# Performance work log

Hardware: AMD Instinct MI355X
Metric: run time of the kernel (lower is better)

## Reference

```python
import jax, jax.numpy as jnp
import numpy as np

NUM_NODES = 20000
LOOKBACK = 7
DAYS = 4
NUM_FEATURES = 5
HIDDEN = 128
NUM_EDGES = 320000


def setup_inputs() -> dict:
    key = jax.random.key(0)
    ks = jax.random.split(key, 10)
    p = lambda k, shape: jax.random.normal(k, shape, dtype=jnp.float32) * 0.1
    return {
        "x": jax.random.normal(ks[0], (DAYS * NUM_NODES, LOOKBACK, NUM_FEATURES), dtype=jnp.float32),
        "edge_index": jax.random.randint(ks[1], (2, NUM_EDGES), 0, NUM_NODES, dtype=jnp.int32),
        "W1": p(ks[2], (NUM_FEATURES, HIDDEN)),
        "b1": jnp.zeros((HIDDEN,), jnp.float32),
        "W2": p(ks[3], (HIDDEN, HIDDEN)),
        "b2": jnp.zeros((HIDDEN,), jnp.float32),
        "W_ih": p(ks[4], (3 * HIDDEN, HIDDEN)),
        "W_hh": p(ks[5], (3 * HIDDEN, HIDDEN)),
        "b_ih": jnp.zeros((3 * HIDDEN,), jnp.float32),
        "b_hh": jnp.zeros((3 * HIDDEN,), jnp.float32),
        "W_out": p(ks[6], (HIDDEN, 5)),
        "b_out": jnp.zeros((5,), jnp.float32),
    }


def reference(x, edge_index, W1, b1, W2, b2, W_ih, W_hh, b_ih, b_hh, W_out, b_out):
    # Eval mode: dropout is identity.
    src, dst = edge_index[0], edge_index[1]
    # GCN symmetric normalization with self-loops: deg includes the self-loop (+1).
    deg = jax.ops.segment_sum(jnp.ones((NUM_EDGES,), jnp.float32), dst, num_segments=NUM_NODES) + 1.0
    dinv = jax.lax.rsqrt(deg)                      # [N]
    norm_e = dinv[src] * dinv[dst]                 # [E] edge norm
    self_norm = 1.0 / deg                          # [N] self-loop norm

    def gcn(h_in, W, b):
        h = h_in @ W                               # [N, C_out]
        msg = h[src] * norm_e[:, None]             # gather + scale  [E, C_out]
        agg = jax.ops.segment_sum(msg, dst, num_segments=NUM_NODES)
        return agg + h * self_norm[:, None] + b

    def gru(xt, h):
        gi = xt @ W_ih.T + b_ih
        gh = h @ W_hh.T + b_hh
        i_r, i_z, i_n = jnp.split(gi, 3, axis=1)
        h_r, h_z, h_n = jnp.split(gh, 3, axis=1)
        r = jax.nn.sigmoid(i_r + h_r)
        z = jax.nn.sigmoid(i_z + h_z)
        n = jnp.tanh(i_n + r * h_n)
        return (1.0 - z) * n + z * h

    def day_fwd(x_day):  # x_day: [N, lookback, F]
        def step(h, xt):
            z1 = jax.nn.relu(gcn(xt, W1, b1))
            z2 = jax.nn.relu(gcn(z1, W2, b2))
            return gru(z2, h), None
        h0 = jnp.zeros((NUM_NODES, HIDDEN), jnp.float32)
        hT, _ = jax.lax.scan(step, h0, jnp.swapaxes(x_day, 0, 1))  # scan over lookback
        return jax.nn.softmax(hT @ W_out + b_out, axis=1)          # [N, 5]

    x_days = x.reshape(DAYS, NUM_NODES, LOOKBACK, NUM_FEATURES)
    out = jax.vmap(day_fwd)(x_days)                # [DAYS, N, 5]
    return out.reshape(DAYS * NUM_NODES, 5)
```

## Files before the change

### kernel.cpp

```cpp
#include <hip/hip_runtime.h>
#include <cstddef>
#include <cstdint>

#define N_NODES 20000
#define N_EDGES 320000
#define NDAYS 4
#define LOOKBACK 7
#define NFEAT 5
#define XROW (LOOKBACK * NFEAT)
#define HIDDEN 128
#define GRUROWS 32

typedef short bf8 __attribute__((ext_vector_type(8)));
typedef float fx4 __attribute__((ext_vector_type(4)));

__device__ __forceinline__ float bflo(unsigned int u) {
    union { unsigned int u; float f; } v; v.u = u << 16; return v.f;
}
__device__ __forceinline__ float bfhi(unsigned int u) {
    union { unsigned int u; float f; } v; v.u = u & 0xffff0000u; return v.f;
}
__device__ __forceinline__ unsigned short f2bf(float f) {
    union { float f; unsigned int u; } v; v.f = f;
    unsigned int u = v.u + 0x7fffu + ((v.u >> 16) & 1u);
    return (unsigned short)(u >> 16);
}
__device__ __forceinline__ unsigned int packbf(float a, float b) {
    return (unsigned int)f2bf(a) | ((unsigned int)f2bf(b) << 16);
}
__device__ __forceinline__ float sigm(float v) { return 1.0f / (1.0f + __expf(-v)); }
__device__ __forceinline__ float ftanh(float v) {
    float e2 = __expf(2.0f * v);
    return (e2 - 1.0f) / (e2 + 1.0f);
}
__device__ __forceinline__ void accum8(float* a, uint4 v, float w) {
    a[0] += w * bflo(v.x); a[1] += w * bfhi(v.x);
    a[2] += w * bflo(v.y); a[3] += w * bfhi(v.y);
    a[4] += w * bflo(v.z); a[5] += w * bfhi(v.z);
    a[6] += w * bflo(v.w); a[7] += w * bfhi(v.w);
}


__global__ __launch_bounds__(256) void k_deg(const int* __restrict__ ei, int* __restrict__ deg) {
    int e = blockIdx.x * 256 + threadIdx.x;
    if (e < N_EDGES) atomicAdd(&deg[ei[N_EDGES + e]], 1);
}

__global__ __launch_bounds__(1024) void k_scan(const int* __restrict__ deg, int* __restrict__ row_start) {
    __shared__ int part[1024];
    int tid = threadIdx.x;
    const int chunk = (N_NODES + 1023) / 1024;
    int i0 = tid * chunk;
    int i1 = min(i0 + chunk, N_NODES);
    int s = 0;
    for (int i = i0; i < i1; ++i) s += deg[i];
    part[tid] = s;
    __syncthreads();
    for (int d = 1; d < 1024; d <<= 1) {
        int v = (tid >= d) ? part[tid - d] : 0;
        __syncthreads();
        part[tid] += v;
        __syncthreads();
    }
    int base = part[tid] - s;
    for (int i = i0; i < i1; ++i) { row_start[i] = base; base += deg[i]; }
    if (tid == 1023) row_start[N_NODES] = part[1023];
}

__global__ __launch_bounds__(256) void k_dinv(const int* __restrict__ deg, float* __restrict__ dinv,
                                              float* __restrict__ self_norm) {
    int i = blockIdx.x * 256 + threadIdx.x;
    if (i >= N_NODES) return;
    float d = (float)(deg[i] + 1);
    dinv[i] = 1.0f / sqrtf(d);
    self_norm[i] = 1.0f / d;
}

__global__ __launch_bounds__(256) void k_fill(const int* __restrict__ ei, const int* __restrict__ row_start,
                                              int* __restrict__ cursor, const float* __restrict__ dinv,
                                              int* __restrict__ csr_src, float* __restrict__ csr_norm) {
    int e = blockIdx.x * 256 + threadIdx.x;
    if (e >= N_EDGES) return;
    int s = ei[e], d = ei[N_EDGES + e];
    int pos = row_start[d] + atomicAdd(&cursor[d], 1);
    csr_src[pos] = s;
    csr_norm[pos] = dinv[s] * dinv[d];
}

__global__ __launch_bounds__(256) void k_w2t(const float* __restrict__ W2, unsigned short* __restrict__ W2T) {
    int idx = blockIdx.x * 256 + threadIdx.x;
    if (idx >= HIDDEN * HIDDEN) return;
    int k = idx >> 7, c = idx & 127;
    W2T[c * HIDDEN + k] = f2bf(W2[k * HIDDEN + c]);
}

__global__ __launch_bounds__(256) void k_cast(const float* __restrict__ src, unsigned short* __restrict__ dst, int n) {
    int i = blockIdx.x * 256 + threadIdx.x;
    if (i < n) dst[i] = f2bf(src[i]);
}

__global__ __launch_bounds__(256) void k_bfold(const float* __restrict__ b_ih, const float* __restrict__ b_hh,
                                               float* __restrict__ b_fold) {
    int i = blockIdx.x * 256 + threadIdx.x;
    if (i < 3 * HIDDEN) b_fold[i] = b_ih[i] + (i < 2 * HIDDEN ? b_hh[i] : 0.0f);
}


template<int NB>
__global__ __launch_bounds__(256) void k_aggx(const float* __restrict__ x, float* __restrict__ xa,
                                              const int* __restrict__ row_start, const int* __restrict__ csr_src,
                                              const float* __restrict__ csr_norm,
                                              const float* __restrict__ self_norm, int dayBase) {
    int n = blockIdx.x * 4 + (threadIdx.x >> 6);
    if (n >= N_NODES) return;
    int lane = threadIdx.x & 63;
    if (lane >= XROW) return;
    float sn = self_norm[n];
    float acc[NB];
#pragma unroll
    for (int b = 0; b < NB; ++b)
        acc[b] = x[(size_t)((dayBase + b) * N_NODES + n) * XROW + lane] * sn;
    int e1 = row_start[n + 1];
    for (int e = row_start[n]; e < e1; ++e) {
        int s = csr_src[e];
        float w = csr_norm[e];
#pragma unroll
        for (int b = 0; b < NB; ++b)
            acc[b] += w * x[(size_t)((dayBase + b) * N_NODES + s) * XROW + lane];
    }
#pragma unroll
    for (int b = 0; b < NB; ++b)
        xa[(size_t)(n * NB + b) * XROW + lane] = acc[b];
}


__global__ __launch_bounds__(256) void k_z1gemm(const float* __restrict__ xa, const float* __restrict__ W1,
                                                const float* __restrict__ b1,
                                                const unsigned short* __restrict__ W2T,
                                                unsigned short* __restrict__ H2, int rows, int t) {
    int tid = threadIdx.x, w = tid >> 6, l = tid & 63, lr = l & 15, lk = l >> 4;
    int rblk = blockIdx.x * 64;
    int rowA = rblk + w * 16 + lr;
    bool okA = rowA < rows;
    float x5[5];
#pragma unroll
    for (int k = 0; k < 5; ++k)
        x5[k] = okA ? xa[(size_t)rowA * XROW + t * NFEAT + k] : 0.0f;
    bf8 az[4];
#pragma unroll
    for (int ks = 0; ks < 4; ++ks) {
#pragma unroll
        for (int j = 0; j < 8; ++j) {
            int ch = 32 * ks + 8 * lk + j;
            float v = b1[ch] + x5[0] * W1[ch] + x5[1] * W1[128 + ch] + x5[2] * W1[256 + ch]
                    + x5[3] * W1[384 + ch] + x5[4] * W1[512 + ch];
            az[ks][j] = (short)f2bf(fmaxf(v, 0.0f));
        }
    }
    const bf8* Bp = (const bf8*)W2T;
    fx4 acc[8];
#pragma unroll
    for (int n = 0; n < 8; ++n) acc[n] = (fx4){0.f, 0.f, 0.f, 0.f};
#pragma unroll
    for (int ks = 0; ks < 4; ++ks) {
#pragma unroll
        for (int n = 0; n < 8; ++n) {
            bf8 b = Bp[(size_t)(16 * n + lr) * 16 + 4 * ks + lk];
            acc[n] = __builtin_amdgcn_mfma_f32_16x16x32_bf16(az[ks], b, acc[n], 0, 0, 0);
        }
    }
#pragma unroll
    for (int n = 0; n < 8; ++n)
#pragma unroll
        for (int r = 0; r < 4; ++r) {
            int row = rblk + w * 16 + lk * 4 + r;
            if (row < rows) H2[(size_t)row * HIDDEN + 16 * n + lr] = f2bf(acc[n][r]);
        }
}


template<int NB>
__global__ __launch_bounds__(256) void k_agg(const uint4* __restrict__ H, uint4* __restrict__ Z,
                                             const float* __restrict__ bias,
                                             const int* __restrict__ row_start, const int* __restrict__ csr_src,
                                             const float* __restrict__ csr_norm,
                                             const float* __restrict__ self_norm) {
    int n = blockIdx.x * 4 + (threadIdx.x >> 6);
    if (n >= N_NODES) return;
    int l = threadIdx.x & 63;
    if (l >= NB * 16) return;
    int c0 = (l & 15) * 8;
    float sn = self_norm[n];
    float a[8];
    {
        uint4 sv = H[(size_t)n * (NB * 16) + l];
        a[0] = bflo(sv.x) * sn; a[1] = bfhi(sv.x) * sn;
        a[2] = bflo(sv.y) * sn; a[3] = bfhi(sv.y) * sn;
        a[4] = bflo(sv.z) * sn; a[5] = bfhi(sv.z) * sn;
        a[6] = bflo(sv.w) * sn; a[7] = bfhi(sv.w) * sn;
    }
    int e1 = row_start[n + 1];
    int e = row_start[n];
    for (; e + 3 < e1; e += 4) {
        int s0 = csr_src[e], s1 = csr_src[e + 1], s2 = csr_src[e + 2], s3 = csr_src[e + 3];
        float w0 = csr_norm[e], w1 = csr_norm[e + 1], w2 = csr_norm[e + 2], w3 = csr_norm[e + 3];
        uint4 v0 = H[(size_t)s0 * (NB * 16) + l];
        uint4 v1 = H[(size_t)s1 * (NB * 16) + l];
        uint4 v2 = H[(size_t)s2 * (NB * 16) + l];
        uint4 v3 = H[(size_t)s3 * (NB * 16) + l];
        accum8(a, v0, w0); accum8(a, v1, w1); accum8(a, v2, w2); accum8(a, v3, w3);
    }
    for (; e < e1; ++e) {
        int s = csr_src[e];
        float w = csr_norm[e];
        uint4 v = H[(size_t)s * (NB * 16) + l];
        accum8(a, v, w);
    }
    const float* bp = bias + c0;
    uint4 o;
    o.x = packbf(fmaxf(a[0] + bp[0], 0.f), fmaxf(a[1] + bp[1], 0.f));
    o.y = packbf(fmaxf(a[2] + bp[2], 0.f), fmaxf(a[3] + bp[3], 0.f));
    o.z = packbf(fmaxf(a[4] + bp[4], 0.f), fmaxf(a[5] + bp[5], 0.f));
    o.w = packbf(fmaxf(a[6] + bp[6], 0.f), fmaxf(a[7] + bp[7], 0.f));
    Z[(size_t)n * (NB * 16) + l] = o;
}


template<bool FIRST>
__global__ __launch_bounds__(512, 1) void k_megagru(const unsigned short* __restrict__ Z2all,
                                                    float* __restrict__ Hf,
                                                    const unsigned short* __restrict__ Wih,
                                                    const unsigned short* __restrict__ Whh,
                                                    const float* __restrict__ bfold,
                                                    const float* __restrict__ bhh, int rows, int NT) {
    __shared__ __align__(16) char hlds[2 * GRUROWS * 256];
    __shared__ __align__(16) char wlds[384 * 256];
    const int HALF = GRUROWS * 256;
    int tid = threadIdx.x, w = tid >> 6, l = tid & 63, lr = l & 15, lk = l >> 4;
    int row0 = blockIdx.x * GRUROWS;
    int c = w * 16 + lr;

    {
        const uint4* wsrc = (const uint4*)Whh;
        for (int i = tid; i < 384 * 16; i += 512) {
            int rw = i >> 4, chunk = i & 15;
            uint4 v = wsrc[(size_t)rw * 16 + chunk];
            int byte = rw * 256 + ((chunk * 16) ^ ((rw & 15) << 4));
            *(uint4*)(wlds + byte) = v;
        }
    }

    bf8 Bi[3][4];
    const bf8* BiP = (const bf8*)Wih;
#pragma unroll
    for (int g = 0; g < 3; ++g)
#pragma unroll
        for (int ks = 0; ks < 4; ++ks)
            Bi[g][ks] = BiP[(size_t)(g * HIDDEN + c) * 16 + 4 * ks + lk];

    float bf_r = bfold[c], bf_z = bfold[HIDDEN + c], bf_n = bfold[2 * HIDDEN + c];
    float bh_n = bhh[2 * HIDDEN + c];

    float hreg[2][4];
    if (FIRST) {
#pragma unroll
        for (int m = 0; m < 2; ++m)
#pragma unroll
            for (int r = 0; r < 4; ++r) hreg[m][r] = 0.f;
        for (int i = tid; i < HALF / 4; i += 512) ((unsigned int*)hlds)[i] = 0u;
    } else {
#pragma unroll
        for (int m = 0; m < 2; ++m)
#pragma unroll
            for (int r = 0; r < 4; ++r) {
                int row = 16 * m + lk * 4 + r;
                float h = Hf[(size_t)(row0 + row) * HIDDEN + c];
                hreg[m][r] = h;
                int byte = row * 256 + ((c * 2) ^ ((row & 15) << 4));
                *(unsigned short*)(hlds + byte) = f2bf(h);
            }
    }
    __syncthreads();

    for (int t = 0; t < NT; ++t) {
        const int p = t & 1;
        const unsigned short* z2t = Z2all + ((size_t)t * rows + row0) * HIDDEN;
#pragma unroll
        for (int m = 0; m < 2; ++m) {
            bf8 az[4];
            const bf8* zp = (const bf8*)(z2t + (size_t)(16 * m + lr) * HIDDEN);
#pragma unroll
            for (int ks = 0; ks < 4; ++ks) az[ks] = zp[4 * ks + lk];
            bf8 ah[4];
#pragma unroll
            for (int ks = 0; ks < 4; ++ks) {
                int byte = p * HALF + (16 * m + lr) * 256 + ((ks * 64 + lk * 16) ^ (lr << 4));
                ah[ks] = *(const bf8*)(hlds + byte);
            }
            fx4 aR = (fx4){0.f, 0.f, 0.f, 0.f};
            fx4 aZ = (fx4){0.f, 0.f, 0.f, 0.f};
            fx4 aNi = (fx4){0.f, 0.f, 0.f, 0.f};
            fx4 aNh = (fx4){0.f, 0.f, 0.f, 0.f};
#pragma unroll
            for (int ks = 0; ks < 4; ++ks) {
                int wb = (ks * 64 + lk * 16) ^ (lr << 4);
                bf8 bhR = *(const bf8*)(wlds + (0 * HIDDEN + c) * 256 + wb);
                bf8 bhZ = *(const bf8*)(wlds + (1 * HIDDEN + c) * 256 + wb);
                bf8 bhN = *(const bf8*)(wlds + (2 * HIDDEN + c) * 256 + wb);
                aR = __builtin_amdgcn_mfma_f32_16x16x32_bf16(ah[ks], bhR, aR, 0, 0, 0);
                aZ = __builtin_amdgcn_mfma_f32_16x16x32_bf16(ah[ks], bhZ, aZ, 0, 0, 0);
                aNh = __builtin_amdgcn_mfma_f32_16x16x32_bf16(ah[ks], bhN, aNh, 0, 0, 0);
            }
#pragma unroll
            for (int ks = 0; ks < 4; ++ks) {
                aR = __builtin_amdgcn_mfma_f32_16x16x32_bf16(az[ks], Bi[0][ks], aR, 0, 0, 0);
                aZ = __builtin_amdgcn_mfma_f32_16x16x32_bf16(az[ks], Bi[1][ks], aZ, 0, 0, 0);
                aNi = __builtin_amdgcn_mfma_f32_16x16x32_bf16(az[ks], Bi[2][ks], aNi, 0, 0, 0);
            }
#pragma unroll
            for (int r = 0; r < 4; ++r) {
                int row = 16 * m + lk * 4 + r;
                float rr = sigm(aR[r] + bf_r);
                float zz = sigm(aZ[r] + bf_z);
                float nn = ftanh(aNi[r] + bf_n + rr * (aNh[r] + bh_n));
                float hnew = (1.0f - zz) * nn + zz * hreg[m][r];
                hreg[m][r] = hnew;
                int byte = (p ^ 1) * HALF + row * 256 + ((c * 2) ^ ((row & 15) << 4));
                *(unsigned short*)(hlds + byte) = f2bf(hnew);
            }
        }
        asm volatile("s_waitcnt lgkmcnt(0)" ::: "memory");
        __builtin_amdgcn_s_barrier();
        __builtin_amdgcn_sched_barrier(0);
    }

#pragma unroll
    for (int m = 0; m < 2; ++m)
#pragma unroll
        for (int r = 0; r < 4; ++r)
            Hf[(size_t)(row0 + 16 * m + lk * 4 + r) * HIDDEN + c] = hreg[m][r];
}


template<int NB>
__global__ __launch_bounds__(256) void k_out(const float* __restrict__ Hc, const float* __restrict__ Wo,
                                             const float* __restrict__ bo, float* __restrict__ out,
                                             int dayBase) {
    int rr = blockIdx.x * 4 + (threadIdx.x >> 6);
    if (rr >= N_NODES * NB) return;
    int lane = threadIdx.x & 63;
    float2 hv = ((const float2*)(Hc + (size_t)rr * HIDDEN))[lane];
    float l[5];
#pragma unroll
    for (int j = 0; j < 5; ++j) {
        float p = hv.x * Wo[(2 * lane) * 5 + j] + hv.y * Wo[(2 * lane + 1) * 5 + j];
#pragma unroll
        for (int s = 1; s < 64; s <<= 1) p += __shfl_xor(p, s);
        l[j] = p + bo[j];
    }
    float m = fmaxf(fmaxf(fmaxf(l[0], l[1]), fmaxf(l[2], l[3])), l[4]);
    float e0 = expf(l[0] - m), e1 = expf(l[1] - m), e2 = expf(l[2] - m), e3 = expf(l[3] - m), e4 = expf(l[4] - m);
    float inv = 1.0f / (e0 + e1 + e2 + e3 + e4);
    if (lane < 5) {
        float ej = lane == 0 ? e0 : lane == 1 ? e1 : lane == 2 ? e2 : lane == 3 ? e3 : e4;
        int n = rr / NB, dd = dayBase + rr % NB;
        out[((size_t)dd * N_NODES + n) * 5 + lane] = ej * inv;
    }
}


template<int NB>
static void run_tier(const float* x, const float* W1, const float* b1,
                     const unsigned short* W2T_bf, const float* b2,
                     const unsigned short* Wih_bf, const unsigned short* Whh_bf,
                     const float* b_fold, const float* b_hh,
                     const float* W_out, const float* b_out, float* out,
                     const int* row_start, const int* csr_src, const float* csr_norm,
                     const float* self_norm,
                     float* xa, unsigned short* H2, unsigned short* Z2all, float* Hf,
                     hipStream_t stream) {
    const int rows = N_NODES * NB;
    const unsigned ngrid = (N_NODES + 3) / 4;
    const unsigned gblk = (unsigned)((rows + 63) / 64);
    const unsigned gru_grid = (unsigned)(rows / GRUROWS);
    const int rounds = NDAYS / NB;
    for (int dd = 0; dd < rounds; ++dd) {
        int dayBase = dd * NB;
        k_aggx<NB><<<ngrid, 256, 0, stream>>>(x, xa, row_start, csr_src, csr_norm, self_norm, dayBase);
        for (int t = 0; t < 4; ++t) {
            k_z1gemm<<<gblk, 256, 0, stream>>>(xa, W1, b1, W2T_bf, H2, rows, t);
            k_agg<NB><<<ngrid, 256, 0, stream>>>((const uint4*)H2,
                                                 (uint4*)(Z2all + (size_t)t * rows * HIDDEN), b2,
                                                 row_start, csr_src, csr_norm, self_norm);
        }
        k_megagru<true><<<gru_grid, 512, 0, stream>>>(Z2all, Hf, Wih_bf, Whh_bf, b_fold, b_hh, rows, 4);
        for (int t = 4; t < LOOKBACK; ++t) {
            k_z1gemm<<<gblk, 256, 0, stream>>>(xa, W1, b1, W2T_bf, H2, rows, t);
            k_agg<NB><<<ngrid, 256, 0, stream>>>((const uint4*)H2,
                                                 (uint4*)(Z2all + (size_t)(t - 4) * rows * HIDDEN), b2,
                                                 row_start, csr_src, csr_norm, self_norm);
        }
        k_megagru<false><<<gru_grid, 512, 0, stream>>>(Z2all, Hf, Wih_bf, Whh_bf, b_fold, b_hh, rows, 3);
        k_out<NB><<<(unsigned)((rows + 3) / 4), 256, 0, stream>>>(Hf, W_out, b_out, out, dayBase);
    }
}


extern "C" void kernel_launch(void* const* d_in, const int* in_sizes, int n_in,
                              void* d_out, int out_size, void* d_ws, size_t ws_size,
                              hipStream_t stream) {
    const float* x     = (const float*)d_in[0];
    const int*   ei    = (const int*)d_in[1];
    const float* W1    = (const float*)d_in[2];
    const float* b1    = (const float*)d_in[3];
    const float* W2    = (const float*)d_in[4];
    const float* b2    = (const float*)d_in[5];
    const float* W_ih  = (const float*)d_in[6];
    const float* W_hh  = (const float*)d_in[7];
    const float* b_ih  = (const float*)d_in[8];
    const float* b_hh  = (const float*)d_in[9];
    const float* W_out = (const float*)d_in[10];
    const float* b_out = (const float*)d_in[11];
    float* out = (float*)d_out;

    size_t off = 0;
    char* wsb = (char*)d_ws;
    auto alloc = [&](size_t bytes) -> void* {
        void* p = wsb + off;
        off = (off + bytes + 255) & ~(size_t)255;
        return p;
    };
    int*            deg       = (int*)alloc(N_NODES * 4);
    int*            cursor    = (int*)alloc(N_NODES * 4);
    int*            row_start = (int*)alloc((N_NODES + 1) * 4);
    float*          dinv      = (float*)alloc(N_NODES * 4);
    float*          self_norm = (float*)alloc(N_NODES * 4);
    unsigned short* W2T_bf    = (unsigned short*)alloc(HIDDEN * HIDDEN * 2);
    unsigned short* Wih_bf    = (unsigned short*)alloc(3 * HIDDEN * HIDDEN * 2);
    unsigned short* Whh_bf    = (unsigned short*)alloc(3 * HIDDEN * HIDDEN * 2);
    float*          b_fold    = (float*)alloc(3 * HIDDEN * 4);
    int*            csr_src   = (int*)alloc(N_EDGES * 4);
    float*          csr_norm  = (float*)alloc(N_EDGES * 4);

    size_t prep_off = off;
    auto need = [&](int nb) -> size_t {
        return prep_off + (size_t)N_NODES * nb * 1932 + 16384;
    };
    int NBsel = (need(4) <= ws_size) ? 4 : (need(2) <= ws_size) ? 2 : 1;
    int rows = N_NODES * NBsel;

    float*          xa    = (float*)alloc((size_t)rows * XROW * 4);
    unsigned short* H2    = (unsigned short*)alloc((size_t)rows * HIDDEN * 2);
    unsigned short* Z2all = (unsigned short*)alloc((size_t)4 * rows * HIDDEN * 2);
    float*          Hf    = (float*)alloc((size_t)rows * HIDDEN * 4);

    hipMemsetAsync(deg, 0, N_NODES * 4, stream);
    hipMemsetAsync(cursor, 0, N_NODES * 4, stream);
    k_deg<<<(N_EDGES + 255) / 256, 256, 0, stream>>>(ei, deg);
    k_scan<<<1, 1024, 0, stream>>>(deg, row_start);
    k_dinv<<<(N_NODES + 255) / 256, 256, 0, stream>>>(deg, dinv, self_norm);
    k_fill<<<(N_EDGES + 255) / 256, 256, 0, stream>>>(ei, row_start, cursor, dinv, csr_src, csr_norm);
    k_w2t<<<(HIDDEN * HIDDEN + 255) / 256, 256, 0, stream>>>(W2, W2T_bf);
    k_cast<<<(3 * HIDDEN * HIDDEN + 255) / 256, 256, 0, stream>>>(W_ih, Wih_bf, 3 * HIDDEN * HIDDEN);
    k_cast<<<(3 * HIDDEN * HIDDEN + 255) / 256, 256, 0, stream>>>(W_hh, Whh_bf, 3 * HIDDEN * HIDDEN);
    k_bfold<<<2, 256, 0, stream>>>(b_ih, b_hh, b_fold);

    if (NBsel == 4)
        run_tier<4>(x, W1, b1, W2T_bf, b2, Wih_bf, Whh_bf, b_fold, b_hh, W_out, b_out, out,
                    row_start, csr_src, csr_norm, self_norm, xa, H2, Z2all, Hf, stream);
    else if (NBsel == 2)
        run_tier<2>(x, W1, b1, W2T_bf, b2, Wih_bf, Whh_bf, b_fold, b_hh, W_out, b_out, out,
                    row_start, csr_src, csr_norm, self_norm, xa, H2, Z2all, Hf, stream);
    else
        run_tier<1>(x, W1, b1, W2T_bf, b2, Wih_bf, Whh_bf, b_fold, b_hh, W_out, b_out, out,
                    row_start, csr_src, csr_norm, self_norm, xa, H2, Z2all, Hf, stream);
}
```

Before: 1.096 ms.

## Double GRU rows per block and hoist W_hh LDS fragments out of row loop

The fused GRU kernel now processes 64 rows per block instead of 32, with bounds guards for a partial last block. The recurrent-weight fragments are read from LDS once per timestep and reused across all four 16-row tiles instead of being reloaded per tile. This cuts LDS traffic and amortizes the per-block W_hh staging, but it raises register pressure (more hreg and 12 extra bf8 fragments) and halves the block count, which may reduce occupancy.

```diff
diff --git a/kernel.cpp b/kernel.cpp
--- a/kernel.cpp
+++ b/kernel.cpp
@@ -9,7 +9,7 @@
 #define NFEAT 5
 #define XROW (LOOKBACK * NFEAT)
 #define HIDDEN 128
-#define GRUROWS 32
+#define GRUROWS 64
 
 typedef short bf8 __attribute__((ext_vector_type(8)));
 typedef float fx4 __attribute__((ext_vector_type(4)));
@@ -261,20 +261,21 @@
     float bf_r = bfold[c], bf_z = bfold[HIDDEN + c], bf_n = bfold[2 * HIDDEN + c];
     float bh_n = bhh[2 * HIDDEN + c];
 
-    float hreg[2][4];
+    float hreg[4][4];
     if (FIRST) {
 #pragma unroll
-        for (int m = 0; m < 2; ++m)
+        for (int m = 0; m < 4; ++m)
 #pragma unroll
             for (int r = 0; r < 4; ++r) hreg[m][r] = 0.f;
         for (int i = tid; i < HALF / 4; i += 512) ((unsigned int*)hlds)[i] = 0u;
     } else {
 #pragma unroll
-        for (int m = 0; m < 2; ++m)
+        for (int m = 0; m < 4; ++m)
 #pragma unroll
             for (int r = 0; r < 4; ++r) {
                 int row = 16 * m + lk * 4 + r;
-                float h = Hf[(size_t)(row0 + row) * HIDDEN + c];
+                int grow = row0 + row;
+                float h = (grow < rows) ? Hf[(size_t)grow * HIDDEN + c] : 0.0f;
                 hreg[m][r] = h;
                 int byte = row * 256 + ((c * 2) ^ ((row & 15) << 4));
                 *(unsigned short*)(hlds + byte) = f2bf(h);
@@ -285,12 +286,25 @@
     for (int t = 0; t < NT; ++t) {
         const int p = t & 1;
         const unsigned short* z2t = Z2all + ((size_t)t * rows + row0) * HIDDEN;
-#pragma unroll
-        for (int m = 0; m < 2; ++m) {
+
+        bf8 bwR[4], bwZ[4], bwN[4];
+#pragma unroll
+        for (int ks = 0; ks < 4; ++ks) {
+            int wb = (ks * 64 + lk * 16) ^ (lr << 4);
+            bwR[ks] = *(const bf8*)(wlds + (0 * HIDDEN + c) * 256 + wb);
+            bwZ[ks] = *(const bf8*)(wlds + (1 * HIDDEN + c) * 256 + wb);
+            bwN[ks] = *(const bf8*)(wlds + (2 * HIDDEN + c) * 256 + wb);
+        }
+
+#pragma unroll
+        for (int m = 0; m < 4; ++m) {
+            int rowA = row0 + 16 * m + lr;
+            bool okA = rowA < rows;
             bf8 az[4];
             const bf8* zp = (const bf8*)(z2t + (size_t)(16 * m + lr) * HIDDEN);
 #pragma unroll
-            for (int ks = 0; ks < 4; ++ks) az[ks] = zp[4 * ks + lk];
+            for (int ks = 0; ks < 4; ++ks)
+                az[ks] = okA ? zp[4 * ks + lk] : (bf8){0, 0, 0, 0, 0, 0, 0, 0};
             bf8 ah[4];
 #pragma unroll
             for (int ks = 0; ks < 4; ++ks) {
@@ -303,13 +317,9 @@
             fx4 aNh = (fx4){0.f, 0.f, 0.f, 0.f};
 #pragma unroll
             for (int ks = 0; ks < 4; ++ks) {
-                int wb = (ks * 64 + lk * 16) ^ (lr << 4);
-                bf8 bhR = *(const bf8*)(wlds + (0 * HIDDEN + c) * 256 + wb);
-                bf8 bhZ = *(const bf8*)(wlds + (1 * HIDDEN + c) * 256 + wb);
-                bf8 bhN = *(const bf8*)(wlds + (2 * HIDDEN + c) * 256 + wb);
-                aR = __builtin_amdgcn_mfma_f32_16x16x32_bf16(ah[ks], bhR, aR, 0, 0, 0);
-                aZ = __builtin_amdgcn_mfma_f32_16x16x32_bf16(ah[ks], bhZ, aZ, 0, 0, 0);
-                aNh = __builtin_amdgcn_mfma_f32_16x16x32_bf16(ah[ks], bhN, aNh, 0, 0, 0);
+                aR = __builtin_amdgcn_mfma_f32_16x16x32_bf16(ah[ks], bwR[ks], aR, 0, 0, 0);
+                aZ = __builtin_amdgcn_mfma_f32_16x16x32_bf16(ah[ks], bwZ[ks], aZ, 0, 0, 0);
+                aNh = __builtin_amdgcn_mfma_f32_16x16x32_bf16(ah[ks], bwN[ks], aNh, 0, 0, 0);
             }
 #pragma unroll
             for (int ks = 0; ks < 4; ++ks) {
@@ -335,10 +345,12 @@
     }
 
 #pragma unroll
-    for (int m = 0; m < 2; ++m)
-#pragma unroll
-        for (int r = 0; r < 4; ++r)
-            Hf[(size_t)(row0 + 16 * m + lk * 4 + r) * HIDDEN + c] = hreg[m][r];
+    for (int m = 0; m < 4; ++m)
+#pragma unroll
+        for (int r = 0; r < 4; ++r) {
+            int grow = row0 + 16 * m + lk * 4 + r;
+            if (grow < rows) Hf[(size_t)grow * HIDDEN + c] = hreg[m][r];
+        }
 }
 
 
@@ -382,7 +394,7 @@
     const int rows = N_NODES * NB;
     const unsigned ngrid = (N_NODES + 3) / 4;
     const unsigned gblk = (unsigned)((rows + 63) / 64);
-    const unsigned gru_grid = (unsigned)(rows / GRUROWS);
+    const unsigned gru_grid = (unsigned)((rows + GRUROWS - 1) / GRUROWS);
     const int rounds = NDAYS / NB;
     for (int dd = 0; dd < rounds; ++dd) {
         int dayBase = dd * NB;
```

Result: faster. 1.006 ms (-8.2%).
